# Performance work log

Measured on AMD Instinct MI355X. Metric: run time of the kernel, lower is better.

## Reference

```python
import jax, jax.numpy as jnp
import numpy as np


def setup_inputs() -> dict:
    key = jax.random.key(0)
    k1, k2, k3 = jax.random.split(key, 3)
    B, S, D = 4, 2048, 1024
    x = jax.random.normal(k1, (B, S, D), dtype=jnp.float32)
    # torch Linear weights: [out_features, in_features]
    w_qkv = jax.random.normal(k2, (3 * D, D), dtype=jnp.float32) * (D ** -0.5)
    w_out = jax.random.normal(k3, (D, D), dtype=jnp.float32) * (D ** -0.5)
    return {"x": x, "w_qkv": w_qkv, "w_out": w_out}


def reference(x, w_qkv, w_out):
    B, S, D = x.shape
    H = 16
    Dh = D // H
    qkv = jnp.einsum("bsd,ed->bse", x, w_qkv)  # [B,S,3D]
    q, k, v = jnp.split(qkv, 3, axis=-1)
    # [B,H,S,Dh]
    q = q.reshape(B, S, H, Dh).transpose(0, 2, 1, 3)
    k = k.reshape(B, S, H, Dh).transpose(0, 2, 1, 3)
    v = v.reshape(B, S, H, Dh).transpose(0, 2, 1, 3)
    scale = 1.0 / jnp.sqrt(jnp.asarray(Dh, dtype=x.dtype))
    scores = jnp.einsum("bhqd,bhkd->bhqk", q, k) * scale
    causal = jnp.tril(jnp.ones((S, S), dtype=bool))
    scores = jnp.where(causal, scores, jnp.finfo(scores.dtype).min)
    attn = jax.nn.softmax(scores, axis=-1)
    out = jnp.einsum("bhqk,bhkd->bhqd", attn, v)
    out = out.transpose(0, 2, 1, 3).reshape(B, S, D)
    return jnp.einsum("bsd,ed->bse", out, w_out)
```

## Files before the change

### kernel.cpp

```cpp
#include <hip/hip_runtime.h>
#include <stdint.h>

typedef __attribute__((ext_vector_type(8))) short short8;
typedef __attribute__((ext_vector_type(4))) float f32x4;
typedef __attribute__((ext_vector_type(16))) float f32x16;
typedef __attribute__((ext_vector_type(4))) unsigned int u32x4;

#define AS1 __attribute__((address_space(1)))
#define AS3 __attribute__((address_space(3)))

#define FSWZ(row) ((((row)) & 7) ^ (((row) >> 3) & 7))

#define KSCL 0.18033688f

__device__ __forceinline__ void gload_lds16(const void* g, void* l) {
  __builtin_amdgcn_global_load_lds((const AS1 void*)g, (AS3 void*)l, 16, 0, 0);
}

__device__ __forceinline__ short f2bf(float f) {
  uint32_t u = __float_as_uint(f);
  u += 0x7fffu + ((u >> 16) & 1u);
  return (short)(u >> 16);
}

__device__ __forceinline__ unsigned int cvtpk(float lo, float hi) {
  unsigned int r;
  asm("v_cvt_pk_bf16_f32 %0, %1, %2" : "=v"(r) : "v"(lo), "v"(hi));
  return r;
}

__global__ __launch_bounds__(256) void cvt_bf16(const float* __restrict__ in,
                                                short* __restrict__ out, int n8) {
  int i = blockIdx.x * 256 + threadIdx.x;
  if (i >= n8) return;
  const float4* p = (const float4*)(in + (size_t)i * 8);
  float4 a = p[0], b = p[1];
  short8 o;
  o[0] = f2bf(a.x); o[1] = f2bf(a.y); o[2] = f2bf(a.z); o[3] = f2bf(a.w);
  o[4] = f2bf(b.x); o[5] = f2bf(b.y); o[6] = f2bf(b.z); o[7] = f2bf(b.w);
  *(short8*)(out + (size_t)i * 8) = o;
}

__global__ __launch_bounds__(256) void gemm_bt(const short* __restrict__ A,
                                               const short* __restrict__ B,
                                               int K, int epi,
                                               short* __restrict__ q,
                                               short* __restrict__ k,
                                               short* __restrict__ v,
                                               float* __restrict__ outF, int N) {
  __shared__ short Al[128 * 64];
  __shared__ short Bl[128 * 64];
  const int tid = threadIdx.x;
  const int lane = tid & 63;
  const int wv = tid >> 6;
  const int wr = wv >> 1, wc = wv & 1;
  const int bm = blockIdx.y * 128, bn = blockIdx.x * 128;
  const int l15 = lane & 15, l4 = lane >> 4;

  f32x4 acc[4][4] = {};

  for (int kt = 0; kt < K; kt += 64) {
#pragma unroll
    for (int i = 0; i < 4; ++i) {
      int c = i * 256 + tid;
      int row = c >> 3, col = (c & 7) * 8;
      gload_lds16(A + (size_t)(bm + row) * K + kt + col, (char*)Al + (size_t)c * 16);
      gload_lds16(B + (size_t)(bn + row) * K + kt + col, (char*)Bl + (size_t)c * 16);
    }
    __syncthreads();
#pragma unroll
    for (int ks = 0; ks < 2; ++ks) {
      short8 af[4], bf[4];
#pragma unroll
      for (int mf = 0; mf < 4; ++mf)
        af[mf] = *(const short8*)&Al[(wr * 64 + mf * 16 + l15) * 64 + ks * 32 + l4 * 8];
#pragma unroll
      for (int nf = 0; nf < 4; ++nf)
        bf[nf] = *(const short8*)&Bl[(wc * 64 + nf * 16 + l15) * 64 + ks * 32 + l4 * 8];
#pragma unroll
      for (int mf = 0; mf < 4; ++mf)
#pragma unroll
        for (int nf = 0; nf < 4; ++nf)
          acc[mf][nf] =
              __builtin_amdgcn_mfma_f32_16x16x32_bf16(af[mf], bf[nf], acc[mf][nf], 0, 0, 0);
    }
    __syncthreads();
  }

  if (epi == 0) {
#pragma unroll
    for (int mf = 0; mf < 4; ++mf)
#pragma unroll
      for (int r = 0; r < 4; ++r) {
        int m = bm + wr * 64 + mf * 16 + l4 * 4 + r;
        int bb = m >> 11, s = m & 2047;
#pragma unroll
        for (int nf = 0; nf < 4; ++nf) {
          int n = bn + wc * 64 + nf * 16 + l15;
          int which = n >> 10, d = n & 1023, h = d >> 6, dh = d & 63;
          short* dst = (which == 0) ? q : ((which == 1) ? k : v);
          float val = acc[mf][nf][r];
          if (which == 1) val *= KSCL;
          dst[((size_t)(bb * 16 + h) * 2048 + s) * 64 + dh] = f2bf(val);
        }
      }
  } else {
#pragma unroll
    for (int mf = 0; mf < 4; ++mf)
#pragma unroll
      for (int r = 0; r < 4; ++r) {
        int m = bm + wr * 64 + mf * 16 + l4 * 4 + r;
#pragma unroll
        for (int nf = 0; nf < 4; ++nf) {
          int n = bn + wc * 64 + nf * 16 + l15;
          outF[(size_t)m * N + n] = acc[mf][nf][r];
        }
      }
  }
}

__global__ __launch_bounds__(256) void attn_fwd(const short* __restrict__ Qb,
                                                const short* __restrict__ Kb,
                                                const short* __restrict__ Vb,
                                                short* __restrict__ Ob) {
  __shared__ short Kl[2][64 * 64];
  __shared__ short Vt[2][64 * 64];
  const int tid = threadIdx.x, lane = tid & 63, wv = tid >> 6;
  const int l31 = lane & 31, l32 = lane >> 5;
  const int bh = blockIdx.x;
  const int qt = (int)gridDim.y - 1 - (int)blockIdx.y;
  const int b = bh >> 4, h = bh & 15;
  const size_t base = (size_t)bh * 2048 * 64;
  const int q0 = qt * 128;
  const int qw0 = q0 + wv * 32;
  const int qg = qw0 + l31;

  short8 qf[4];
#pragma unroll
  for (int dk = 0; dk < 4; ++dk)
    qf[dk] = *(const short8*)(Qb + base + (size_t)qg * 64 + dk * 16 + l32 * 8);

  f32x16 oacc[2] = {};
  float mrun = -1e30f, lrun = 0.f;
  short8 vv[2];

  const int nt = 2 * qt + 2;
#pragma unroll
  for (int i = 0; i < 2; ++i) {
    int c = i * 256 + tid;
    int row = c >> 3, j = c & 7;
    gload_lds16(Kb + base + (size_t)row * 64 + (j ^ FSWZ(row)) * 8,
                (char*)Kl[0] + (size_t)c * 16);
    vv[i] = *(const short8*)(Vb + base + (size_t)(c >> 3) * 64 + (c & 7) * 8);
  }

  for (int t = 0; t < nt; ++t) {
    const int cur = t & 1;
    const int kv0 = t * 64;
#pragma unroll
    for (int i = 0; i < 2; ++i) {
      int c = i * 256 + tid;
      int kr = c >> 3, c0 = (c & 7) * 8;
#pragma unroll
      for (int j = 0; j < 8; ++j) {
        int vr = c0 + j;
        Vt[cur][vr * 64 + (((kr >> 3) ^ FSWZ(vr)) * 8) + (kr & 7)] = vv[i][j];
      }
    }
    __syncthreads();

    if (t + 1 < nt) {
      const int kv1 = kv0 + 64;
#pragma unroll
      for (int i = 0; i < 2; ++i) {
        int c = i * 256 + tid;
        int row = c >> 3, j = c & 7;
        gload_lds16(Kb + base + (size_t)(kv1 + row) * 64 + (j ^ FSWZ(row)) * 8,
                    (char*)Kl[cur ^ 1] + (size_t)c * 16);
        vv[i] = *(const short8*)(Vb + base + (size_t)(kv1 + (c >> 3)) * 64 + (c & 7) * 8);
      }
    }

    if (kv0 <= qw0 + 31) {
      f32x16 sc[2] = {};
      __builtin_amdgcn_s_setprio(1);
#pragma unroll
      for (int dk = 0; dk < 4; ++dk)
#pragma unroll
        for (int kb = 0; kb < 2; ++kb) {
          int row = kb * 32 + l31;
          short8 kf =
              *(const short8*)&Kl[cur][row * 64 + (((dk * 2 + l32) ^ FSWZ(row)) * 8)];
          sc[kb] = __builtin_amdgcn_mfma_f32_32x32x16_bf16(kf, qf[dk], sc[kb], 0, 0, 0);
        }
      __builtin_amdgcn_s_setprio(0);

      const bool diag = (kv0 + 63 > qw0);
      float pp[2][16];
#pragma unroll
      for (int kb = 0; kb < 2; ++kb)
#pragma unroll
        for (int r = 0; r < 16; ++r) {
          float s = sc[kb][r];
          if (diag) {
            int kgl = kv0 + kb * 32 + (r & 3) + 8 * (r >> 2) + 4 * l32;
            if (kgl > qg) s = -1e30f;
          }
          pp[kb][r] = s;
        }
      float mx = -1e30f;
#pragma unroll
      for (int kb = 0; kb < 2; ++kb)
#pragma unroll
        for (int r = 0; r < 16; ++r) mx = fmaxf(mx, pp[kb][r]);
      mx = fmaxf(mx, __shfl_xor(mx, 32));
      if (!__all(mx - mrun <= 11.5416f)) {
        float mnew = fmaxf(mrun, mx);
        float alpha = exp2f(mrun - mnew);
        lrun *= alpha;
#pragma unroll
        for (int dt = 0; dt < 2; ++dt)
#pragma unroll
          for (int r = 0; r < 16; ++r) oacc[dt][r] *= alpha;
        mrun = mnew;
      }
      float ls = 0.f;
#pragma unroll
      for (int kb = 0; kb < 2; ++kb)
#pragma unroll
        for (int r = 0; r < 16; ++r) {
          float e = exp2f(pp[kb][r] - mrun);
          pp[kb][r] = e;
          ls += e;
        }
      ls += __shfl_xor(ls, 32);
      lrun += ls;

      unsigned int W[2][4][2];
#pragma unroll
      for (int kb = 0; kb < 2; ++kb)
#pragma unroll
        for (int g = 0; g < 4; ++g)
#pragma unroll
          for (int u = 0; u < 2; ++u)
            W[kb][g][u] = cvtpk(pp[kb][g * 4 + 2 * u], pp[kb][g * 4 + 2 * u + 1]);

      u32x4 pf[4];
#pragma unroll
      for (int kblk = 0; kblk < 4; ++kblk) {
        const int kbh = kblk >> 1;
#pragma unroll
        for (int u = 0; u < 2; ++u) {
          unsigned int A = W[kbh][2 * (kblk & 1)][u];
          unsigned int B = W[kbh][2 * (kblk & 1) + 1][u];
          unsigned int own = l32 ? B : A;
          unsigned int snd = l32 ? A : B;
          unsigned int rcv = (unsigned int)__shfl_xor((int)snd, 32);
          pf[kblk][0 + u] = l32 ? rcv : own;
          pf[kblk][2 + u] = l32 ? own : rcv;
        }
      }

      __builtin_amdgcn_s_setprio(1);
#pragma unroll
      for (int dt = 0; dt < 2; ++dt)
#pragma unroll
        for (int kblk = 0; kblk < 4; ++kblk) {
          int row = dt * 32 + l31;
          short8 vf =
              *(const short8*)&Vt[cur][row * 64 + (((kblk * 2 + l32) ^ FSWZ(row)) * 8)];
          oacc[dt] = __builtin_amdgcn_mfma_f32_32x32x16_bf16(
              vf, __builtin_bit_cast(short8, pf[kblk]), oacc[dt], 0, 0, 0);
        }
      __builtin_amdgcn_s_setprio(0);
    }
  }

  float inv = 1.f / lrun;
#pragma unroll
  for (int dt = 0; dt < 2; ++dt)
#pragma unroll
    for (int r = 0; r < 16; ++r) {
      int d = dt * 32 + (r & 3) + 8 * (r >> 2) + 4 * l32;
      Ob[(size_t)(b * 2048 + qg) * 1024 + h * 64 + d] = f2bf(oacc[dt][r] * inv);
    }
}

extern "C" void kernel_launch(void* const* d_in, const int* in_sizes, int n_in,
                              void* d_out, int out_size, void* d_ws, size_t ws_size,
                              hipStream_t stream) {
  const float* x = (const float*)d_in[0];
  const float* w_qkv = (const float*)d_in[1];
  const float* w_out = (const float*)d_in[2];
  float* out = (float*)d_out;

  char* ws = (char*)d_ws;
  const size_t MB = 1024 * 1024;
  short* xb    = (short*)(ws + 0 * MB);
  short* wqkvb = (short*)(ws + 16 * MB);
  short* woutb = (short*)(ws + 22 * MB);
  short* qb    = (short*)(ws + 24 * MB);
  short* kb    = (short*)(ws + 40 * MB);
  short* vb    = (short*)(ws + 56 * MB);
  short* ao    = xb;

  cvt_bf16<<<4096, 256, 0, stream>>>(x, xb, 8192 * 1024 / 8);
  cvt_bf16<<<1536, 256, 0, stream>>>(w_qkv, wqkvb, 3072 * 1024 / 8);
  cvt_bf16<<<512, 256, 0, stream>>>(w_out, woutb, 1024 * 1024 / 8);

  gemm_bt<<<dim3(3072 / 128, 8192 / 128), 256, 0, stream>>>(
      xb, wqkvb, 1024, 0, qb, kb, vb, nullptr, 3072);

  attn_fwd<<<dim3(64, 16), 256, 0, stream>>>(qb, kb, vb, ao);

  gemm_bt<<<dim3(1024 / 128, 8192 / 128), 256, 0, stream>>>(
      ao, woutb, 1024, 1, nullptr, nullptr, nullptr, out, 1024);
}
```

Before: 224.4 us.

## Merge conversion kernels, swizzle GEMM blocks across XCDs, drop setprio in attention

Replaces the three fp32-to-bf16 conversion launches with one kernel that picks its source and destination by thread index, saving two launches. Remaps the GEMM block index so consecutive blocks are spread across the 8 XCDs, which is intended to improve L2 locality of the A and B tiles. Removes the s_setprio bracketing around the MFMA sections in the attention kernel, which changes wave scheduling priority. Each of these is independent and small, and the priority change could help or hurt overlap.

```diff
diff --git a/kernel.cpp b/kernel.cpp
--- a/kernel.cpp
+++ b/kernel.cpp
@@ -29,16 +29,33 @@
   return r;
 }
 
-__global__ __launch_bounds__(256) void cvt_bf16(const float* __restrict__ in,
-                                                short* __restrict__ out, int n8) {
+__global__ __launch_bounds__(256) void cvt_all(const float* __restrict__ x,
+                                               const float* __restrict__ wq,
+                                               const float* __restrict__ wo,
+                                               short* __restrict__ xb,
+                                               short* __restrict__ wqb,
+                                               short* __restrict__ wob) {
   int i = blockIdx.x * 256 + threadIdx.x;
-  if (i >= n8) return;
-  const float4* p = (const float4*)(in + (size_t)i * 8);
+  const float* in;
+  short* out;
+  if (i < 1048576) {
+    in = x + (size_t)i * 8;
+    out = xb + (size_t)i * 8;
+  } else if (i < 1441792) {
+    int j = i - 1048576;
+    in = wq + (size_t)j * 8;
+    out = wqb + (size_t)j * 8;
+  } else {
+    int j = i - 1441792;
+    in = wo + (size_t)j * 8;
+    out = wob + (size_t)j * 8;
+  }
+  const float4* p = (const float4*)in;
   float4 a = p[0], b = p[1];
   short8 o;
   o[0] = f2bf(a.x); o[1] = f2bf(a.y); o[2] = f2bf(a.z); o[3] = f2bf(a.w);
   o[4] = f2bf(b.x); o[5] = f2bf(b.y); o[6] = f2bf(b.z); o[7] = f2bf(b.w);
-  *(short8*)(out + (size_t)i * 8) = o;
+  *(short8*)out = o;
 }
 
 __global__ __launch_bounds__(256) void gemm_bt(const short* __restrict__ A,
@@ -54,7 +71,11 @@
   const int lane = tid & 63;
   const int wv = tid >> 6;
   const int wr = wv >> 1, wc = wv & 1;
-  const int bm = blockIdx.y * 128, bn = blockIdx.x * 128;
+  const int gx = gridDim.x;
+  const int lin = blockIdx.y * gx + blockIdx.x;
+  const int cpx = (gx * gridDim.y) >> 3;
+  const int swz = (lin & 7) * cpx + (lin >> 3);
+  const int bm = (swz / gx) * 128, bn = (swz % gx) * 128;
   const int l15 = lane & 15, l4 = lane >> 4;
 
   f32x4 acc[4][4] = {};
@@ -183,7 +204,6 @@
 
     if (kv0 <= qw0 + 31) {
       f32x16 sc[2] = {};
-      __builtin_amdgcn_s_setprio(1);
 #pragma unroll
       for (int dk = 0; dk < 4; ++dk)
 #pragma unroll
@@ -193,7 +213,6 @@
               *(const short8*)&Kl[cur][row * 64 + (((dk * 2 + l32) ^ FSWZ(row)) * 8)];
           sc[kb] = __builtin_amdgcn_mfma_f32_32x32x16_bf16(kf, qf[dk], sc[kb], 0, 0, 0);
         }
-      __builtin_amdgcn_s_setprio(0);
 
       const bool diag = (kv0 + 63 > qw0);
       float pp[2][16];
@@ -261,7 +280,6 @@
         }
       }
 
-      __builtin_amdgcn_s_setprio(1);
 #pragma unroll
       for (int dt = 0; dt < 2; ++dt)
 #pragma unroll
@@ -272,7 +290,6 @@
           oacc[dt] = __builtin_amdgcn_mfma_f32_32x32x16_bf16(
               vf, __builtin_bit_cast(short8, pf[kblk]), oacc[dt], 0, 0, 0);
         }
-      __builtin_amdgcn_s_setprio(0);
     }
   }
 
@@ -304,9 +321,7 @@
   short* vb    = (short*)(ws + 56 * MB);
   short* ao    = xb;
 
-  cvt_bf16<<<4096, 256, 0, stream>>>(x, xb, 8192 * 1024 / 8);
-  cvt_bf16<<<1536, 256, 0, stream>>>(w_qkv, wqkvb, 3072 * 1024 / 8);
-  cvt_bf16<<<512, 256, 0, stream>>>(w_out, woutb, 1024 * 1024 / 8);
+  cvt_all<<<6144, 256, 0, stream>>>(x, w_qkv, w_out, xb, wqkvb, woutb);
 
   gemm_bt<<<dim3(3072 / 128, 8192 / 128), 256, 0, stream>>>(
       xb, wqkvb, 1024, 0, qb, kb, vb, nullptr, 3072);
```

Result: no change. 223.8 us (-0.3%).
